# Kernel optimization log

Measured on AMD Instinct MI355X. Metric: run time of the kernel, lower is better.

The kernel has to match this reference:

```python
import jax, jax.numpy as jnp
import numpy as np

KERNEL_SIZE = 9
HEAD_SIZE = 64


def setup_inputs() -> dict:
    key = jax.random.key(0)
    k1, k2 = jax.random.split(key)
    B, S, D = 8, 4096, 768          # hidden = num_heads(12) * head_size(64)
    H = D // HEAD_SIZE              # 12 heads
    inputs = jax.random.normal(k1, (B, S, D), dtype=jnp.float32)
    filters = jax.random.normal(k2, (B, S, H * KERNEL_SIZE), dtype=jnp.float32)
    return {"inputs": inputs, "filters": filters}


def reference(inputs, filters):
    k = KERNEL_SIZE
    hd = HEAD_SIZE
    bs, S, d = inputs.shape
    H = d // hd
    pad = k // 2
    # softmax-normalized per-(position, head) kernels: [B, S, H, k]
    f = jax.nn.softmax(filters.reshape(bs, S, H, k), axis=-1)
    # 'same' padding along sequence, then gather sliding windows (im2col)
    x = jnp.pad(inputs, ((0, 0), (pad, pad), (0, 0)))        # [B, S+k-1, d]
    idx = jnp.arange(S)[:, None] + jnp.arange(k)[None, :]     # [S, k]
    win = x[:, idx].reshape(bs, S, k, H, hd)                  # [B, S, k, H, hd]
    # dynamic depthwise conv: contract kernel taps per head
    out = jnp.einsum('bskhd,bshk->bshd', win, f)              # [B, S, H, hd]
    return out
```

## Files before the change

### kernel.cpp

```cpp
#include <hip/hip_runtime.h>
#include <math.h>


#define KS 9
#define HD 64
#define NH 12
#define DMODEL 768
#define SEQ 4096
#define BATCH 8
#define TTILE 16
#define CHUNKS (SEQ / TTILE)
#define FSTRIDE (NH * KS)
#define NTHREADS 192

__global__ __launch_bounds__(NTHREADS, 6) void lightconv_kernel(
    const float* __restrict__ x,
    const float* __restrict__ filt,
    float* __restrict__ out)
{
    __shared__ float wlds[TTILE * FSTRIDE];

    const int blk   = blockIdx.x;
    const int chunk = blk & (CHUNKS - 1);
    const int b     = blk >> 8;
    const int s0    = chunk * TTILE;
    const int t     = threadIdx.x;

    const float* fbase = filt + ((size_t)b * SEQ + s0) * FSTRIDE;
#pragma unroll
    for (int i = 0; i < (TTILE * FSTRIDE) / NTHREADS; ++i) {
        const int idx = t + i * NTHREADS;
        wlds[idx] = fbase[idx];
    }
    __syncthreads();

    {
        const int sl = t & 15;
        const int hh = t >> 4;
        float* wp = &wlds[sl * FSTRIDE + hh * KS];
        float w[KS];
        float m = -1e30f;
#pragma unroll
        for (int k = 0; k < KS; ++k) { w[k] = wp[k]; m = fmaxf(m, w[k]); }
        float sum = 0.f;
#pragma unroll
        for (int k = 0; k < KS; ++k) { w[k] = __expf(w[k] - m); sum += w[k]; }
        const float inv = 1.0f / sum;
#pragma unroll
        for (int k = 0; k < KS; ++k) wp[k] = w[k] * inv;
    }
    __syncthreads();

    const int head = t >> 4;
    const int d4   = (t & 15) << 2;

    const float* xc = x   + (size_t)b * SEQ * DMODEL + head * HD + d4;
    float*       oc = out + (size_t)b * SEQ * DMODEL + head * HD + d4;

    const float4 zero = make_float4(0.f, 0.f, 0.f, 0.f);

    float4 win[KS];
#pragma unroll
    for (int k = 0; k < KS - 1; ++k) {
        const int ss = s0 + k - (KS / 2);
        win[k] = (ss >= 0) ? *reinterpret_cast<const float4*>(xc + (size_t)ss * DMODEL)
                           : zero;
    }

#pragma unroll
    for (int i = 0; i < TTILE; ++i) {
        const int s  = s0 + i;
        const int ss = s + (KS / 2);
        win[KS - 1] = (ss < SEQ) ? *reinterpret_cast<const float4*>(xc + (size_t)ss * DMODEL)
                                 : zero;

        const float* wp = &wlds[i * FSTRIDE + head * KS];

        float4 acc = zero;
#pragma unroll
        for (int k = 0; k < KS; ++k) {
            const float wk = wp[k];
            acc.x += wk * win[k].x;
            acc.y += wk * win[k].y;
            acc.z += wk * win[k].z;
            acc.w += wk * win[k].w;
        }
        *reinterpret_cast<float4*>(oc + (size_t)s * DMODEL) = acc;

#pragma unroll
        for (int k = 0; k < KS - 1; ++k) win[k] = win[k + 1];
    }
}

extern "C" void kernel_launch(void* const* d_in, const int* in_sizes, int n_in,
                              void* d_out, int out_size, void* d_ws, size_t ws_size,
                              hipStream_t stream) {
    const float* x    = (const float*)d_in[0];
    const float* filt = (const float*)d_in[1];
    float* out        = (float*)d_out;

    const int grid = BATCH * CHUNKS;
    lightconv_kernel<<<grid, NTHREADS, 0, stream>>>(x, filt, out);
}
```

Baseline: 192.7 us.

## Prefetch all input rows into registers before softmax to overlap loads

Issues all 24 input row loads and the filter loads into registers up front, before the filter softmax and its barriers, so global memory latency overlaps with the softmax work instead of being exposed inside the compute loop. The sliding-window shift is replaced by a fully unrolled register array. Occupancy hint drops from 6 to 4 blocks per CU to fit the larger register footprint, which reduces latency hiding across waves.

```diff
diff --git a/kernel.cpp b/kernel.cpp
--- a/kernel.cpp
+++ b/kernel.cpp
@@ -9,11 +9,12 @@
 #define SEQ 4096
 #define BATCH 8
 #define TTILE 16
+#define NROWS (TTILE + KS - 1)
 #define CHUNKS (SEQ / TTILE)
 #define FSTRIDE (NH * KS)
 #define NTHREADS 192
 
-__global__ __launch_bounds__(NTHREADS, 6) void lightconv_kernel(
+__global__ __launch_bounds__(NTHREADS, 4) void lightconv_kernel(
     const float* __restrict__ x,
     const float* __restrict__ filt,
     float* __restrict__ out)
@@ -25,13 +26,28 @@
     const int b     = blk >> 8;
     const int s0    = chunk * TTILE;
     const int t     = threadIdx.x;
+    const int head  = t >> 4;
+    const int d4    = (t & 15) << 2;
+
+    const float4 zero = make_float4(0.f, 0.f, 0.f, 0.f);
 
     const float* fbase = filt + ((size_t)b * SEQ + s0) * FSTRIDE;
+    float freg[KS];
 #pragma unroll
-    for (int i = 0; i < (TTILE * FSTRIDE) / NTHREADS; ++i) {
-        const int idx = t + i * NTHREADS;
-        wlds[idx] = fbase[idx];
+    for (int i = 0; i < KS; ++i) freg[i] = fbase[t + i * NTHREADS];
+
+    const float* xc = x + (size_t)b * SEQ * DMODEL + head * HD + d4;
+    float4 rows[NROWS];
+#pragma unroll
+    for (int r = 0; r < NROWS; ++r) {
+        const int ss = s0 + r - (KS / 2);
+        rows[r] = (ss >= 0 && ss < SEQ)
+                    ? *reinterpret_cast<const float4*>(xc + (size_t)ss * DMODEL)
+                    : zero;
     }
+
+#pragma unroll
+    for (int i = 0; i < KS; ++i) wlds[t + i * NTHREADS] = freg[i];
     __syncthreads();
 
     {
@@ -51,44 +67,20 @@
     }
     __syncthreads();
 
-    const int head = t >> 4;
-    const int d4   = (t & 15) << 2;
-
-    const float* xc = x   + (size_t)b * SEQ * DMODEL + head * HD + d4;
-    float*       oc = out + (size_t)b * SEQ * DMODEL + head * HD + d4;
-
-    const float4 zero = make_float4(0.f, 0.f, 0.f, 0.f);
-
-    float4 win[KS];
-#pragma unroll
-    for (int k = 0; k < KS - 1; ++k) {
-        const int ss = s0 + k - (KS / 2);
-        win[k] = (ss >= 0) ? *reinterpret_cast<const float4*>(xc + (size_t)ss * DMODEL)
-                           : zero;
-    }
-
+    float* oc = out + (size_t)b * SEQ * DMODEL + head * HD + d4;
 #pragma unroll
     for (int i = 0; i < TTILE; ++i) {
-        const int s  = s0 + i;
-        const int ss = s + (KS / 2);
-        win[KS - 1] = (ss < SEQ) ? *reinterpret_cast<const float4*>(xc + (size_t)ss * DMODEL)
-                                 : zero;
-
         const float* wp = &wlds[i * FSTRIDE + head * KS];
-
         float4 acc = zero;
 #pragma unroll
         for (int k = 0; k < KS; ++k) {
             const float wk = wp[k];
-            acc.x += wk * win[k].x;
-            acc.y += wk * win[k].y;
-            acc.z += wk * win[k].z;
-            acc.w += wk * win[k].w;
+            acc.x += wk * rows[i + k].x;
+            acc.y += wk * rows[i + k].y;
+            acc.z += wk * rows[i + k].z;
+            acc.w += wk * rows[i + k].w;
         }
-        *reinterpret_cast<float4*>(oc + (size_t)s * DMODEL) = acc;
-
-#pragma unroll
-        for (int k = 0; k < KS - 1; ++k) win[k] = win[k + 1];
+        *reinterpret_cast<float4*>(oc + (size_t)(s0 + i) * DMODEL) = acc;
     }
 }
 
```

Result: no change. 195.1 us (+1.2%).
